# Optimization experiments

Measured on AMD Instinct MI355X. Metric: run time of the kernel, lower is better.

Reference implementation:

```python
import jax, jax.numpy as jnp
import numpy as np

K = 128
D = 256
N = 8192


def setup_inputs() -> dict:
    key = jax.random.key(0)
    k1, k2, k3, k4, k5 = jax.random.split(key, 5)
    x = jax.random.normal(k1, (N, D), dtype=jnp.float32)
    means = jax.random.uniform(k2, (K, D), dtype=jnp.float32)
    diag = 1.0 + 0.1 * jax.random.normal(k3, (1, K, D), dtype=jnp.float32)
    tri = 0.01 * jax.random.normal(k4, (1, K, D, D), dtype=jnp.float32)
    weigh = jax.random.normal(k5, (1, K), dtype=jnp.float32)
    return {"x": x, "means": means, "diag": diag, "tri": tri, "weigh": weigh}


def reference(x, means, diag, tri, weigh):
    # logC = -d/2 * log(2*pi)
    logC = jnp.asarray(-D / 2 * np.log(2 * np.pi), dtype=x.dtype)
    w = jax.nn.log_softmax(weigh, axis=1)            # [1, K]
    y = x[:, None, :] - means                        # [N, K, d]
    tril = jnp.tril(tri[0], k=-1)                    # [K, d, d] (strictly lower)
    # y * diag + batched tril matvec per component
    y = y * diag + jnp.einsum('kde,nke->nkd', tril, y)
    s = jnp.sum(y * y, axis=2)                       # [N, K]
    lp = -s / 2 + jnp.sum(jnp.log(jnp.abs(diag)), axis=2) + w  # [N, K]
    lp = jax.scipy.special.logsumexp(lp, axis=-1)    # [N]
    logpdf = logC + lp
    return jnp.mean(jnp.abs(-logpdf))
```

## Files before the change

### kernel.cpp

```cpp
#include <hip/hip_runtime.h>
#include <hip/hip_bf16.h>

#define DN   256
#define KC   128
#define NTOT 8192

typedef __attribute__((ext_vector_type(4)))  float f32x4;
typedef __attribute__((ext_vector_type(16))) float f32x16;
typedef __attribute__((ext_vector_type(4)))  unsigned int u32x4;
typedef __attribute__((ext_vector_type(8)))  int i32x8;

__device__ __forceinline__ unsigned pk4(float a0, float a1, float a2, float a3) {
  int v = __builtin_amdgcn_cvt_pk_fp8_f32(a0, a1, 0, false);
  v = __builtin_amdgcn_cvt_pk_fp8_f32(a2, a3, v, true);
  return (unsigned)v;
}
__device__ __forceinline__ float rt8(float v) {
  int p = __builtin_amdgcn_cvt_pk_fp8_f32(v, v, 0, false);
  return __builtin_amdgcn_cvt_f32_fp8(p, 0);
}

__device__ __forceinline__ void gload16(const void* g, void* l) {
  __builtin_amdgcn_global_load_lds(
      (const __attribute__((address_space(1))) unsigned int*)g,
      (__attribute__((address_space(3))) unsigned int*)l, 16, 0, 0);
}

__device__ __forceinline__ void inv_gran(int gi, int& r, int& g) {
  int l2 = gi >> 3, slot = gi & 7;
  int ss = slot ^ (l2 & 7);
  r = 2 * l2 + (ss >> 2);
  g = ss & 3;
}

__global__ void gmm_const(const float* __restrict__ diag,
                          const float* __restrict__ weigh,
                          float* __restrict__ ck) {
  int k = blockIdx.x;
  int lane = threadIdx.x;
  float w0 = weigh[lane], w1 = weigh[64 + lane];
  float mx = fmaxf(w0, w1);
#pragma unroll
  for (int off = 32; off > 0; off >>= 1) mx = fmaxf(mx, __shfl_xor(mx, off, 64));
  float s = expf(w0 - mx) + expf(w1 - mx);
#pragma unroll
  for (int off = 32; off > 0; off >>= 1) s += __shfl_xor(s, off, 64);
  float lse = mx + logf(s);
  float ld = 0.f;
  const float* dp = diag + (size_t)k * DN;
#pragma unroll
  for (int j = 0; j < 4; ++j) ld += logf(fabsf(dp[lane + 64 * j]));
#pragma unroll
  for (int off = 32; off > 0; off >>= 1) ld += __shfl_xor(ld, off, 64);
  if (lane == 0) ck[k] = ld + weigh[k] - lse;
}

__global__ void gmm_cvec(const float* __restrict__ tri,
                         const float* __restrict__ diag,
                         const float* __restrict__ means,
                         float* __restrict__ C) {
  int k  = blockIdx.x >> 2;
  int d0 = (blockIdx.x & 3) * 64;
  int lane = threadIdx.x & 63;
  int wid  = threadIdx.x >> 6;
  for (int i = 0; i < 16; ++i) {
    int d = d0 + wid * 16 + i;
    const float* trow = tri + (((size_t)k) << 16) + (d << 8);
    float dg = diag[(k << 8) + d];
    float acc = 0.f;
#pragma unroll
    for (int eb = 0; eb < DN; eb += 64) {
      int e = eb + lane;
      float mv = (e < d) ? trow[e] : ((e == d) ? dg : 0.f);
      acc += rt8(mv) * means[(k << 8) + e];
    }
#pragma unroll
    for (int off = 32; off > 0; off >>= 1) acc += __shfl_xor(acc, off, 64);
    if (lane == 0) C[(k << 8) + d] = acc;
  }
}

__global__ void gmm_packA(const float* __restrict__ x,
                          unsigned char* __restrict__ Xp) {
  int t = blockIdx.x * 256 + threadIdx.x;
  int rb = t >> 12;
  int rem = t & 4095;
  int tc = rem >> 10;
  int gi = rem & 1023;
  int r, g; inv_gran(gi, r, g);
  int row = rb * 256 + r;
  int e0 = tc * 64 + g * 16;
  const float* src = x + (size_t)row * DN + e0;
  float4 v0 = *(const float4*)src;
  float4 v1 = *(const float4*)(src + 4);
  float4 v2 = *(const float4*)(src + 8);
  float4 v3 = *(const float4*)(src + 12);
  u32x4 o = {pk4(v0.x, v0.y, v0.z, v0.w), pk4(v1.x, v1.y, v1.z, v1.w),
             pk4(v2.x, v2.y, v2.z, v2.w), pk4(v3.x, v3.y, v3.z, v3.w)};
  *(u32x4*)(Xp + (size_t)t * 16) = o;
}

__global__ void gmm_packB(const float* __restrict__ tri,
                          const float* __restrict__ diag,
                          unsigned char* __restrict__ Mp) {
  int t = blockIdx.x * 256 + threadIdx.x;
  int k = t >> 12;
  int rem = t & 4095;
  int tc = rem >> 10;
  int r2 = rem & 1023;
  int dhh = r2 >> 9;
  int gi = r2 & 511;
  int r, g; inv_gran(gi, r, g);
  int d = dhh * 128 + r;
  int e0 = tc * 64 + g * 16;
  const float* src = tri + (((size_t)k) << 16) + (d << 8) + e0;
  float dg = diag[(k << 8) + d];
  float4 v0 = *(const float4*)src;
  float4 v1 = *(const float4*)(src + 4);
  float4 v2 = *(const float4*)(src + 8);
  float4 v3 = *(const float4*)(src + 12);
  float f[16] = {v0.x, v0.y, v0.z, v0.w, v1.x, v1.y, v1.z, v1.w,
                 v2.x, v2.y, v2.z, v2.w, v3.x, v3.y, v3.z, v3.w};
#pragma unroll
  for (int j = 0; j < 16; ++j) {
    int e = e0 + j;
    f[j] = (e < d) ? f[j] : ((e == d) ? dg : 0.f);
  }
  u32x4 o = {pk4(f[0], f[1], f[2], f[3]), pk4(f[4], f[5], f[6], f[7]),
             pk4(f[8], f[9], f[10], f[11]), pk4(f[12], f[13], f[14], f[15])};
  *(u32x4*)(Mp + (size_t)t * 16) = o;
}

template <int USEP>
__global__ __launch_bounds__(512, 4) void gmm_gemm(
    const float* __restrict__ x, const float* __restrict__ tri,
    const float* __restrict__ diag, const unsigned char* __restrict__ Xp,
    const unsigned char* __restrict__ Mp, const float* __restrict__ C,
    float* __restrict__ Sp) {
  __shared__ __attribute__((aligned(16))) unsigned char As[3][8192];
  __shared__ __attribute__((aligned(16))) unsigned char Bs[3][16384];
  __shared__ float C_lds[128];
  __shared__ float spart[256][2];

  const int tid  = threadIdx.x;
  const int lane = tid & 63;
  const int wid  = tid >> 6;
  const int wm   = wid >> 1;
  const int wn   = wid & 1;
  const int l31  = lane & 31;
  const int h    = lane >> 5;

  const int bid = blockIdx.x;
  const int xcd = bid & 7;
  const int j   = bid >> 3;
  const int k   = xcd * 16 + (j & 15);
  const int u   = j >> 4;
  const int dh  = u & 1;
  const int rb  = u >> 1;
  const int NT  = 2 + 2 * dh;

  f32x16 acc[2][2];
#pragma unroll
  for (int df = 0; df < 2; ++df)
#pragma unroll
    for (int nf = 0; nf < 2; ++nf)
#pragma unroll
      for (int q = 0; q < 16; ++q) acc[df][nf][q] = 0.f;

  const int rA = wn * 32 + l31, lA = rA >> 1;
  const int rB = wm * 64 + l31, lB = rB >> 1;
  const int aoff0 = lA * 128 + (((2 * h)     + 4 * (rA & 1)) ^ (lA & 7)) * 16;
  const int aoff1 = lA * 128 + (((2 * h + 1) + 4 * (rA & 1)) ^ (lA & 7)) * 16;
  const int boff0 = lB * 128 + (((2 * h)     + 4 * (rB & 1)) ^ (lB & 7)) * 16;
  const int boff1 = lB * 128 + (((2 * h + 1) + 4 * (rB & 1)) ^ (lB & 7)) * 16;

  auto stage = [&](int ring, int tc) {
    gload16(Mp + (((size_t)((k * 4 + tc) * 2 + dh)) * 512 + tid) * 16,
            &As[ring][wid * 1024]);
    const unsigned char* gb = Xp + (((size_t)(rb * 4 + tc)) * 1024 + tid) * 16;
    gload16(gb, &Bs[ring][wid * 1024]);
    gload16(gb + 512 * 16, &Bs[ring][8192 + wid * 1024]);
  };

  auto compute = [&](int ring, int t) {
    const char* Ab = (const char*)&As[ring][0];
    const char* Bb = (const char*)&Bs[ring][0];
    u32x4 xlo[2], xhi[2];
#pragma unroll
    for (int nf = 0; nf < 2; ++nf) {
      xlo[nf] = *(const u32x4*)(Bb + boff0 + nf * 2048);
      xhi[nf] = *(const u32x4*)(Bb + boff1 + nf * 2048);
    }
#pragma unroll
    for (int df = 0; df < 2; ++df) {
      if (2 * dh + df >= t) {
        u32x4 m0 = *(const u32x4*)(Ab + aoff0 + df * 4096);
        u32x4 m1 = *(const u32x4*)(Ab + aoff1 + df * 4096);
        i32x8 ma;
#pragma unroll
        for (int q = 0; q < 4; ++q) { ma[q] = (int)m0[q]; ma[4 + q] = (int)m1[q]; }
#pragma unroll
        for (int nf = 0; nf < 2; ++nf) {
          i32x8 xb;
#pragma unroll
          for (int q = 0; q < 4; ++q) { xb[q] = (int)xlo[nf][q]; xb[4 + q] = (int)xhi[nf][q]; }
          acc[df][nf] = __builtin_amdgcn_mfma_scale_f32_32x32x64_f8f6f4(
              ma, xb, acc[df][nf], 0, 0, 0, 0x7f7f7f7f, 0, 0x7f7f7f7f);
        }
      }
    }
  };

  if (tid < 128) C_lds[tid] = C[(k << 8) + dh * 128 + tid];
  __syncthreads();

  if (USEP) {
    stage(0, 0); stage(1, 1);
    int rc = 0;
    for (int t = 0; t < NT; ++t) {
      if (t + 2 < NT) { int rs = rc + 2; if (rs >= 3) rs -= 3; stage(rs, t + 2); }
      int infl = NT - 1 - t; if (infl > 2) infl = 2;
      if (infl == 2)      asm volatile("s_waitcnt vmcnt(6)" ::: "memory");
      else if (infl == 1) asm volatile("s_waitcnt vmcnt(3)" ::: "memory");
      else                asm volatile("s_waitcnt vmcnt(0)" ::: "memory");
      __builtin_amdgcn_s_barrier();
      __builtin_amdgcn_sched_barrier(0);
      compute(rc, t);
      __builtin_amdgcn_s_barrier();
      __builtin_amdgcn_sched_barrier(0);
      if (++rc == 3) rc = 0;
    }
  } else {
    int rc = 0;
    for (int t = 0; t < NT; ++t) {
      __syncthreads();
      {
        int r, g; inv_gran(tid & 511, r, g);
        if (tid < 512) {
          int d = dh * 128 + r;
          int e0 = t * 64 + g * 16;
          const float* st = tri + (((size_t)k) << 16) + (d << 8) + e0;
          float dg = diag[(k << 8) + d];
          float f[16];
#pragma unroll
          for (int jj = 0; jj < 16; ++jj) {
            int e = e0 + jj;
            f[jj] = (e < d) ? st[jj] : ((e == d) ? dg : 0.f);
          }
          u32x4 o = {pk4(f[0], f[1], f[2], f[3]), pk4(f[4], f[5], f[6], f[7]),
                     pk4(f[8], f[9], f[10], f[11]), pk4(f[12], f[13], f[14], f[15])};
          *(u32x4*)&As[rc][(tid & 511) * 16] = o;
        }
      }
#pragma unroll
      for (int i = 0; i < 2; ++i) {
        int gi = i * 512 + tid;
        int r, g; inv_gran(gi, r, g);
        int row = rb * 256 + r;
        int e0 = t * 64 + g * 16;
        const float* sx = x + ((size_t)row << 8) + e0;
        float4 v0 = *(const float4*)sx;
        float4 v1 = *(const float4*)(sx + 4);
        float4 v2 = *(const float4*)(sx + 8);
        float4 v3 = *(const float4*)(sx + 12);
        u32x4 o = {pk4(v0.x, v0.y, v0.z, v0.w), pk4(v1.x, v1.y, v1.z, v1.w),
                   pk4(v2.x, v2.y, v2.z, v2.w), pk4(v3.x, v3.y, v3.z, v3.w)};
        *(u32x4*)&Bs[rc][gi * 16] = o;
      }
      __syncthreads();
      compute(rc, t);
      if (++rc == 3) rc = 0;
    }
    __syncthreads();
  }

  float s0 = 0.f, s1 = 0.f;
#pragma unroll
  for (int df = 0; df < 2; ++df)
#pragma unroll
    for (int qg = 0; qg < 4; ++qg) {
      f32x4 cv = *(const f32x4*)&C_lds[df * 64 + wn * 32 + qg * 8 + 4 * h];
#pragma unroll
      for (int qi = 0; qi < 4; ++qi) {
        int q = qg * 4 + qi;
        float z0 = acc[df][0][q] - cv[qi];
        float z1 = acc[df][1][q] - cv[qi];
        s0 += z0 * z0;
        s1 += z1 * z1;
      }
    }
  s0 += __shfl_xor(s0, 32, 64);
  s1 += __shfl_xor(s1, 32, 64);
  if (lane < 32) {
    spart[wm * 64 + l31][wn]      = s0;
    spart[wm * 64 + 32 + l31][wn] = s1;
  }
  __syncthreads();
  if (tid < 256)
    Sp[((size_t)(dh * KC + k)) * NTOT + rb * 256 + tid] =
        spart[tid][0] + spart[tid][1];
}

__global__ void gmm_lse(const float* __restrict__ Sp,
                        const float* __restrict__ ck,
                        float* __restrict__ out) {
  int n = blockIdx.x * 256 + threadIdx.x;
  float m = -1e30f, s = 0.f;
#pragma unroll 4
  for (int kk = 0; kk < KC; ++kk) {
    float sv = Sp[(size_t)kk * NTOT + n] + Sp[(size_t)(KC + kk) * NTOT + n];
    float v = ck[kk] - 0.5f * sv;
    float nm = fmaxf(m, v);
    s = s * expf(m - nm) + expf(v - nm);
    m = nm;
  }
  float lse = m + logf(s);
  const float logC = -(DN * 0.5f) * 1.8378770664093453f;
  float val = fabsf(logC + lse) * (1.0f / (float)NTOT);
  int lane = threadIdx.x & 63;
  int wid  = threadIdx.x >> 6;
#pragma unroll
  for (int off = 32; off > 0; off >>= 1) val += __shfl_down(val, off, 64);
  __shared__ float wsum[4];
  if (lane == 0) wsum[wid] = val;
  __syncthreads();
  if (threadIdx.x == 0)
    atomicAdd(out, wsum[0] + wsum[1] + wsum[2] + wsum[3]);
}

extern "C" void kernel_launch(void* const* d_in, const int* in_sizes, int n_in,
                              void* d_out, int out_size, void* d_ws, size_t ws_size,
                              hipStream_t stream) {
  const float* x     = (const float*)d_in[0];
  const float* means = (const float*)d_in[1];
  const float* diag  = (const float*)d_in[2];
  const float* tri   = (const float*)d_in[3];
  const float* weigh = (const float*)d_in[4];
  float* out = (float*)d_out;

  char* ws = (char*)d_ws;
  size_t off_ck = 0;
  size_t off_C  = 1024;
  size_t off_Sp = off_C + (size_t)KC * DN * 4;
  size_t off_Xp = off_Sp + (size_t)2 * KC * NTOT * 4;
  size_t off_Mp = off_Xp + (size_t)NTOT * DN;
  size_t need   = off_Mp + (size_t)KC * DN * DN;
  int useP = (ws_size >= need) ? 1 : 0;

  float* ck = (float*)(ws + off_ck);
  float* C  = (float*)(ws + off_C);
  float* Sp = (float*)(ws + off_Sp);
  unsigned char* Xp = (unsigned char*)(ws + off_Xp);
  unsigned char* Mp = (unsigned char*)(ws + off_Mp);

  hipMemsetAsync(d_out, 0, sizeof(float), stream);
  gmm_const<<<KC, 64, 0, stream>>>(diag, weigh, ck);
  gmm_cvec<<<KC * 4, 256, 0, stream>>>(tri, diag, means, C);
  if (useP) {
    gmm_packB<<<(KC * 4 * 2 * 512) / 256, 256, 0, stream>>>(tri, diag, Mp);
    gmm_packA<<<(32 * 4 * 1024) / 256, 256, 0, stream>>>(x, Xp);
    gmm_gemm<1><<<8192, 512, 0, stream>>>(x, tri, diag, Xp, Mp, C, Sp);
  } else {
    gmm_gemm<0><<<8192, 512, 0, stream>>>(x, tri, diag, Xp, Mp, C, Sp);
  }
  gmm_lse<<<NTOT / 256, 256, 0, stream>>>(Sp, ck, out);
}
```

Before: 116.6 us.

## Fuse prep kernels into one launch and compute C from packed fp8 tiles

```diff
diff --git a/kernel.cpp b/kernel.cpp
--- a/kernel.cpp
+++ b/kernel.cpp
@@ -33,102 +33,92 @@
   g = ss & 3;
 }
 
-__global__ void gmm_const(const float* __restrict__ diag,
-                          const float* __restrict__ weigh,
-                          float* __restrict__ ck) {
-  int k = blockIdx.x;
-  int lane = threadIdx.x;
-  float w0 = weigh[lane], w1 = weigh[64 + lane];
-  float mx = fmaxf(w0, w1);
-#pragma unroll
-  for (int off = 32; off > 0; off >>= 1) mx = fmaxf(mx, __shfl_xor(mx, off, 64));
-  float s = expf(w0 - mx) + expf(w1 - mx);
-#pragma unroll
-  for (int off = 32; off > 0; off >>= 1) s += __shfl_xor(s, off, 64);
-  float lse = mx + logf(s);
-  float ld = 0.f;
-  const float* dp = diag + (size_t)k * DN;
-#pragma unroll
-  for (int j = 0; j < 4; ++j) ld += logf(fabsf(dp[lane + 64 * j]));
-#pragma unroll
-  for (int off = 32; off > 0; off >>= 1) ld += __shfl_xor(ld, off, 64);
-  if (lane == 0) ck[k] = ld + weigh[k] - lse;
-}
-
-__global__ void gmm_cvec(const float* __restrict__ tri,
-                         const float* __restrict__ diag,
-                         const float* __restrict__ means,
-                         float* __restrict__ C) {
-  int k  = blockIdx.x >> 2;
-  int d0 = (blockIdx.x & 3) * 64;
-  int lane = threadIdx.x & 63;
-  int wid  = threadIdx.x >> 6;
-  for (int i = 0; i < 16; ++i) {
-    int d = d0 + wid * 16 + i;
-    const float* trow = tri + (((size_t)k) << 16) + (d << 8);
-    float dg = diag[(k << 8) + d];
-    float acc = 0.f;
-#pragma unroll
-    for (int eb = 0; eb < DN; eb += 64) {
-      int e = eb + lane;
-      float mv = (e < d) ? trow[e] : ((e == d) ? dg : 0.f);
-      acc += rt8(mv) * means[(k << 8) + e];
-    }
-#pragma unroll
-    for (int off = 32; off > 0; off >>= 1) acc += __shfl_xor(acc, off, 64);
-    if (lane == 0) C[(k << 8) + d] = acc;
-  }
-}
-
-__global__ void gmm_packA(const float* __restrict__ x,
-                          unsigned char* __restrict__ Xp) {
-  int t = blockIdx.x * 256 + threadIdx.x;
-  int rb = t >> 12;
-  int rem = t & 4095;
-  int tc = rem >> 10;
-  int gi = rem & 1023;
-  int r, g; inv_gran(gi, r, g);
-  int row = rb * 256 + r;
-  int e0 = tc * 64 + g * 16;
-  const float* src = x + (size_t)row * DN + e0;
-  float4 v0 = *(const float4*)src;
-  float4 v1 = *(const float4*)(src + 4);
-  float4 v2 = *(const float4*)(src + 8);
-  float4 v3 = *(const float4*)(src + 12);
-  u32x4 o = {pk4(v0.x, v0.y, v0.z, v0.w), pk4(v1.x, v1.y, v1.z, v1.w),
-             pk4(v2.x, v2.y, v2.z, v2.w), pk4(v3.x, v3.y, v3.z, v3.w)};
-  *(u32x4*)(Xp + (size_t)t * 16) = o;
-}
-
-__global__ void gmm_packB(const float* __restrict__ tri,
-                          const float* __restrict__ diag,
-                          unsigned char* __restrict__ Mp) {
-  int t = blockIdx.x * 256 + threadIdx.x;
-  int k = t >> 12;
-  int rem = t & 4095;
-  int tc = rem >> 10;
-  int r2 = rem & 1023;
-  int dhh = r2 >> 9;
-  int gi = r2 & 511;
-  int r, g; inv_gran(gi, r, g);
-  int d = dhh * 128 + r;
-  int e0 = tc * 64 + g * 16;
-  const float* src = tri + (((size_t)k) << 16) + (d << 8) + e0;
-  float dg = diag[(k << 8) + d];
-  float4 v0 = *(const float4*)src;
-  float4 v1 = *(const float4*)(src + 4);
-  float4 v2 = *(const float4*)(src + 8);
-  float4 v3 = *(const float4*)(src + 12);
-  float f[16] = {v0.x, v0.y, v0.z, v0.w, v1.x, v1.y, v1.z, v1.w,
-                 v2.x, v2.y, v2.z, v2.w, v3.x, v3.y, v3.z, v3.w};
-#pragma unroll
-  for (int j = 0; j < 16; ++j) {
-    int e = e0 + j;
-    f[j] = (e < d) ? f[j] : ((e == d) ? dg : 0.f);
-  }
-  u32x4 o = {pk4(f[0], f[1], f[2], f[3]), pk4(f[4], f[5], f[6], f[7]),
-             pk4(f[8], f[9], f[10], f[11]), pk4(f[12], f[13], f[14], f[15])};
-  *(u32x4*)(Mp + (size_t)t * 16) = o;
+__global__ __launch_bounds__(256) void gmm_prep(
+    const float* __restrict__ x, const float* __restrict__ tri,
+    const float* __restrict__ diag, const float* __restrict__ means,
+    const float* __restrict__ weigh,
+    unsigned char* __restrict__ Xp, unsigned char* __restrict__ Mp,
+    float* __restrict__ C, float* __restrict__ ck) {
+  int b = blockIdx.x;
+  if (b < 2048) {
+    int t = b * 256 + (int)threadIdx.x;
+    int k = t >> 12;
+    int rem = t & 4095;
+    int tc = rem >> 10;
+    int r2 = rem & 1023;
+    int dhh = r2 >> 9;
+    int gi = r2 & 511;
+    int r, g; inv_gran(gi, r, g);
+    int d = dhh * 128 + r;
+    int e0 = tc * 64 + g * 16;
+    if (e0 > d) {
+      u32x4 o = {0u, 0u, 0u, 0u};
+      *(u32x4*)(Mp + (size_t)t * 16) = o;
+    } else {
+      const float* src = tri + (((size_t)k) << 16) + (d << 8) + e0;
+      float dg = diag[(k << 8) + d];
+      float4 v0 = *(const float4*)src;
+      float4 v1 = *(const float4*)(src + 4);
+      float4 v2 = *(const float4*)(src + 8);
+      float4 v3 = *(const float4*)(src + 12);
+      float f[16] = {v0.x, v0.y, v0.z, v0.w, v1.x, v1.y, v1.z, v1.w,
+                     v2.x, v2.y, v2.z, v2.w, v3.x, v3.y, v3.z, v3.w};
+#pragma unroll
+      for (int jj = 0; jj < 16; ++jj) {
+        int e = e0 + jj;
+        f[jj] = (e < d) ? f[jj] : ((e == d) ? dg : 0.f);
+      }
+      u32x4 o = {pk4(f[0], f[1], f[2], f[3]), pk4(f[4], f[5], f[6], f[7]),
+                 pk4(f[8], f[9], f[10], f[11]), pk4(f[12], f[13], f[14], f[15])};
+      *(u32x4*)(Mp + (size_t)t * 16) = o;
+      float part = 0.f;
+      const float* mrow = means + (k << 8) + e0;
+#pragma unroll
+      for (int w = 0; w < 4; ++w) {
+        float4 mv = *(const float4*)(mrow + 4 * w);
+        part += __builtin_amdgcn_cvt_f32_fp8((int)o[w], 0) * mv.x;
+        part += __builtin_amdgcn_cvt_f32_fp8((int)o[w], 1) * mv.y;
+        part += __builtin_amdgcn_cvt_f32_fp8((int)o[w], 2) * mv.z;
+        part += __builtin_amdgcn_cvt_f32_fp8((int)o[w], 3) * mv.w;
+      }
+      atomicAdd(&C[(k << 8) + d], part);
+    }
+  } else if (b < 2560) {
+    int t = (b - 2048) * 256 + (int)threadIdx.x;
+    int rb = t >> 12;
+    int rem = t & 4095;
+    int tc = rem >> 10;
+    int gi = rem & 1023;
+    int r, g; inv_gran(gi, r, g);
+    int row = rb * 256 + r;
+    int e0 = tc * 64 + g * 16;
+    const float* src = x + (size_t)row * DN + e0;
+    float4 v0 = *(const float4*)src;
+    float4 v1 = *(const float4*)(src + 4);
+    float4 v2 = *(const float4*)(src + 8);
+    float4 v3 = *(const float4*)(src + 12);
+    u32x4 o = {pk4(v0.x, v0.y, v0.z, v0.w), pk4(v1.x, v1.y, v1.z, v1.w),
+               pk4(v2.x, v2.y, v2.z, v2.w), pk4(v3.x, v3.y, v3.z, v3.w)};
+    *(u32x4*)(Xp + (size_t)t * 16) = o;
+  } else {
+    int lane = (int)threadIdx.x & 63;
+    int kk = (b - 2560) * 4 + ((int)threadIdx.x >> 6);
+    float w0 = weigh[lane], w1 = weigh[64 + lane];
+    float mx = fmaxf(w0, w1);
+#pragma unroll
+    for (int off = 32; off > 0; off >>= 1) mx = fmaxf(mx, __shfl_xor(mx, off, 64));
+    float s = expf(w0 - mx) + expf(w1 - mx);
+#pragma unroll
+    for (int off = 32; off > 0; off >>= 1) s += __shfl_xor(s, off, 64);
+    float lse = mx + logf(s);
+    float ld = 0.f;
+    const float* dp = diag + (size_t)kk * DN;
+#pragma unroll
+    for (int jj = 0; jj < 4; ++jj) ld += logf(fabsf(dp[lane + 64 * jj]));
+#pragma unroll
+    for (int off = 32; off > 0; off >>= 1) ld += __shfl_xor(ld, off, 64);
+    if (lane == 0) ck[kk] = ld + weigh[kk] - lse;
+  }
 }
 
 template <int USEP>
@@ -328,6 +318,53 @@
     atomicAdd(out, wsum[0] + wsum[1] + wsum[2] + wsum[3]);
 }
 
+__global__ void gmm_const(const float* __restrict__ diag,
+                          const float* __restrict__ weigh,
+                          float* __restrict__ ck) {
+  int k = blockIdx.x;
+  int lane = threadIdx.x;
+  float w0 = weigh[lane], w1 = weigh[64 + lane];
+  float mx = fmaxf(w0, w1);
+#pragma unroll
+  for (int off = 32; off > 0; off >>= 1) mx = fmaxf(mx, __shfl_xor(mx, off, 64));
+  float s = expf(w0 - mx) + expf(w1 - mx);
+#pragma unroll
+  for (int off = 32; off > 0; off >>= 1) s += __shfl_xor(s, off, 64);
+  float lse = mx + logf(s);
+  float ld = 0.f;
+  const float* dp = diag + (size_t)k * DN;
+#pragma unroll
+  for (int j = 0; j < 4; ++j) ld += logf(fabsf(dp[lane + 64 * j]));
+#pragma unroll
+  for (int off = 32; off > 0; off >>= 1) ld += __shfl_xor(ld, off, 64);
+  if (lane == 0) ck[k] = ld + weigh[k] - lse;
+}
+
+__global__ void gmm_cvec(const float* __restrict__ tri,
+                         const float* __restrict__ diag,
+                         const float* __restrict__ means,
+                         float* __restrict__ C) {
+  int k  = blockIdx.x >> 2;
+  int d0 = (blockIdx.x & 3) * 64;
+  int lane = threadIdx.x & 63;
+  int wid  = threadIdx.x >> 6;
+  for (int i = 0; i < 16; ++i) {
+    int d = d0 + wid * 16 + i;
+    const float* trow = tri + (((size_t)k) << 16) + (d << 8);
+    float dg = diag[(k << 8) + d];
+    float acc = 0.f;
+#pragma unroll
+    for (int eb = 0; eb < DN; eb += 64) {
+      int e = eb + lane;
+      float mv = (e < d) ? trow[e] : ((e == d) ? dg : 0.f);
+      acc += rt8(mv) * means[(k << 8) + e];
+    }
+#pragma unroll
+    for (int off = 32; off > 0; off >>= 1) acc += __shfl_xor(acc, off, 64);
+    if (lane == 0) C[(k << 8) + d] = acc;
+  }
+}
+
 extern "C" void kernel_launch(void* const* d_in, const int* in_sizes, int n_in,
                               void* d_out, int out_size, void* d_ws, size_t ws_size,
                               hipStream_t stream) {
@@ -354,13 +391,13 @@
   unsigned char* Mp = (unsigned char*)(ws + off_Mp);
 
   hipMemsetAsync(d_out, 0, sizeof(float), stream);
-  gmm_const<<<KC, 64, 0, stream>>>(diag, weigh, ck);
-  gmm_cvec<<<KC * 4, 256, 0, stream>>>(tri, diag, means, C);
   if (useP) {
-    gmm_packB<<<(KC * 4 * 2 * 512) / 256, 256, 0, stream>>>(tri, diag, Mp);
-    gmm_packA<<<(32 * 4 * 1024) / 256, 256, 0, stream>>>(x, Xp);
+    hipMemsetAsync(C, 0, (size_t)KC * DN * 4, stream);
+    gmm_prep<<<2592, 256, 0, stream>>>(x, tri, diag, means, weigh, Xp, Mp, C, ck);
     gmm_gemm<1><<<8192, 512, 0, stream>>>(x, tri, diag, Xp, Mp, C, Sp);
   } else {
+    gmm_const<<<KC, 64, 0, stream>>>(diag, weigh, ck);
+    gmm_cvec<<<KC * 4, 256, 0, stream>>>(tri, diag, means, C);
     gmm_gemm<0><<<8192, 512, 0, stream>>>(x, tri, diag, Xp, Mp, C, Sp);
   }
   gmm_lse<<<NTOT / 256, 256, 0, stream>>>(Sp, ck, out);
```

Measured after the change: 124.6 us. 6.9% more time.

## Merge both d-halves into one block to reuse X tiles across full D

Applied to the files above, without the earlier changes.

```diff
diff --git a/kernel.cpp b/kernel.cpp
--- a/kernel.cpp
+++ b/kernel.cpp
@@ -113,6 +113,11 @@
   int r, g; inv_gran(gi, r, g);
   int d = dhh * 128 + r;
   int e0 = tc * 64 + g * 16;
+  if (e0 > d) {
+    u32x4 o = {0u, 0u, 0u, 0u};
+    *(u32x4*)(Mp + (size_t)t * 16) = o;
+    return;
+  }
   const float* src = tri + (((size_t)k) << 16) + (d << 8) + e0;
   float dg = diag[(k << 8) + d];
   float4 v0 = *(const float4*)src;
@@ -132,21 +137,21 @@
 }
 
 template <int USEP>
-__global__ __launch_bounds__(512, 4) void gmm_gemm(
+__global__ __launch_bounds__(512, 2) void gmm_gemm(
     const float* __restrict__ x, const float* __restrict__ tri,
     const float* __restrict__ diag, const unsigned char* __restrict__ Xp,
     const unsigned char* __restrict__ Mp, const float* __restrict__ C,
     float* __restrict__ Sp) {
-  __shared__ __attribute__((aligned(16))) unsigned char As[3][8192];
+  __shared__ __attribute__((aligned(16))) unsigned char As[3][16384];
   __shared__ __attribute__((aligned(16))) unsigned char Bs[3][16384];
-  __shared__ float C_lds[128];
+  __shared__ float C_lds[256];
   __shared__ float spart[256][2];
 
   const int tid  = threadIdx.x;
   const int lane = tid & 63;
   const int wid  = tid >> 6;
   const int wm   = wid >> 1;
-  const int wn   = wid & 1;
+  const int ws   = wid & 1;
   const int l31  = lane & 31;
   const int h    = lane >> 5;
 
@@ -154,20 +159,18 @@
   const int xcd = bid & 7;
   const int j   = bid >> 3;
   const int k   = xcd * 16 + (j & 15);
-  const int u   = j >> 4;
-  const int dh  = u & 1;
-  const int rb  = u >> 1;
-  const int NT  = 2 + 2 * dh;
-
-  f32x16 acc[2][2];
-#pragma unroll
-  for (int df = 0; df < 2; ++df)
+  const int rb  = j >> 4;
+  const int NT  = 4;
+
+  f32x16 acc[4][2];
+#pragma unroll
+  for (int fi = 0; fi < 4; ++fi)
 #pragma unroll
     for (int nf = 0; nf < 2; ++nf)
 #pragma unroll
-      for (int q = 0; q < 16; ++q) acc[df][nf][q] = 0.f;
-
-  const int rA = wn * 32 + l31, lA = rA >> 1;
+      for (int q = 0; q < 16; ++q) acc[fi][nf][q] = 0.f;
+
+  const int rA = ws * 32 + l31, lA = rA >> 1;
   const int rB = wm * 64 + l31, lB = rB >> 1;
   const int aoff0 = lA * 128 + (((2 * h)     + 4 * (rA & 1)) ^ (lA & 7)) * 16;
   const int aoff1 = lA * 128 + (((2 * h + 1) + 4 * (rA & 1)) ^ (lA & 7)) * 16;
@@ -175,11 +178,12 @@
   const int boff1 = lB * 128 + (((2 * h + 1) + 4 * (rB & 1)) ^ (lB & 7)) * 16;
 
   auto stage = [&](int ring, int tc) {
-    gload16(Mp + (((size_t)((k * 4 + tc) * 2 + dh)) * 512 + tid) * 16,
-            &As[ring][wid * 1024]);
+    const unsigned char* ga = Mp + (((size_t)(k * 4 + tc)) * 1024 + tid) * 16;
+    gload16(ga, &As[ring][wid * 1024]);
+    gload16(ga + 8192, &As[ring][8192 + wid * 1024]);
     const unsigned char* gb = Xp + (((size_t)(rb * 4 + tc)) * 1024 + tid) * 16;
     gload16(gb, &Bs[ring][wid * 1024]);
-    gload16(gb + 512 * 16, &Bs[ring][8192 + wid * 1024]);
+    gload16(gb + 8192, &Bs[ring][8192 + wid * 1024]);
   };
 
   auto compute = [&](int ring, int t) {
@@ -192,10 +196,10 @@
       xhi[nf] = *(const u32x4*)(Bb + boff1 + nf * 2048);
     }
 #pragma unroll
-    for (int df = 0; df < 2; ++df) {
-      if (2 * dh + df >= t) {
-        u32x4 m0 = *(const u32x4*)(Ab + aoff0 + df * 4096);
-        u32x4 m1 = *(const u32x4*)(Ab + aoff1 + df * 4096);
+    for (int fi = 0; fi < 4; ++fi) {
+      if (fi >= t) {
+        u32x4 m0 = *(const u32x4*)(Ab + aoff0 + fi * 4096);
+        u32x4 m1 = *(const u32x4*)(Ab + aoff1 + fi * 4096);
         i32x8 ma;
 #pragma unroll
         for (int q = 0; q < 4; ++q) { ma[q] = (int)m0[q]; ma[4 + q] = (int)m1[q]; }
@@ -204,14 +208,14 @@
           i32x8 xb;
 #pragma unroll
           for (int q = 0; q < 4; ++q) { xb[q] = (int)xlo[nf][q]; xb[4 + q] = (int)xhi[nf][q]; }
-          acc[df][nf] = __builtin_amdgcn_mfma_scale_f32_32x32x64_f8f6f4(
-              ma, xb, acc[df][nf], 0, 0, 0, 0x7f7f7f7f, 0, 0x7f7f7f7f);
+          acc[fi][nf] = __builtin_amdgcn_mfma_scale_f32_32x32x64_f8f6f4(
+              ma, xb, acc[fi][nf], 0, 0, 0, 0x7f7f7f7f, 0, 0x7f7f7f7f);
         }
       }
     }
   };
 
-  if (tid < 128) C_lds[tid] = C[(k << 8) + dh * 128 + tid];
+  if (tid < 256) C_lds[tid] = C[(k << 8) + tid];
   __syncthreads();
 
   if (USEP) {
@@ -220,8 +224,8 @@
     for (int t = 0; t < NT; ++t) {
       if (t + 2 < NT) { int rs = rc + 2; if (rs >= 3) rs -= 3; stage(rs, t + 2); }
       int infl = NT - 1 - t; if (infl > 2) infl = 2;
-      if (infl == 2)      asm volatile("s_waitcnt vmcnt(6)" ::: "memory");
-      else if (infl == 1) asm volatile("s_waitcnt vmcnt(3)" ::: "memory");
+      if (infl == 2)      asm volatile("s_waitcnt vmcnt(8)" ::: "memory");
+      else if (infl == 1) asm volatile("s_waitcnt vmcnt(4)" ::: "memory");
       else                asm volatile("s_waitcnt vmcnt(0)" ::: "memory");
       __builtin_amdgcn_s_barrier();
       __builtin_amdgcn_sched_barrier(0);
@@ -234,23 +238,29 @@
     int rc = 0;
     for (int t = 0; t < NT; ++t) {
       __syncthreads();
-      {
-        int r, g; inv_gran(tid & 511, r, g);
-        if (tid < 512) {
-          int d = dh * 128 + r;
-          int e0 = t * 64 + g * 16;
+#pragma unroll
+      for (int i = 0; i < 2; ++i) {
+        int gi = i * 512 + tid;
+        int half = gi >> 9;
+        int r, g; inv_gran(gi & 511, r, g);
+        int d = half * 128 + r;
+        int e0 = t * 64 + g * 16;
+        float f[16];
+        if (e0 > d) {
+#pragma unroll
+          for (int jj = 0; jj < 16; ++jj) f[jj] = 0.f;
+        } else {
           const float* st = tri + (((size_t)k) << 16) + (d << 8) + e0;
           float dg = diag[(k << 8) + d];
-          float f[16];
 #pragma unroll
           for (int jj = 0; jj < 16; ++jj) {
             int e = e0 + jj;
             f[jj] = (e < d) ? st[jj] : ((e == d) ? dg : 0.f);
           }
-          u32x4 o = {pk4(f[0], f[1], f[2], f[3]), pk4(f[4], f[5], f[6], f[7]),
-                     pk4(f[8], f[9], f[10], f[11]), pk4(f[12], f[13], f[14], f[15])};
-          *(u32x4*)&As[rc][(tid & 511) * 16] = o;
         }
+        u32x4 o = {pk4(f[0], f[1], f[2], f[3]), pk4(f[4], f[5], f[6], f[7]),
+                   pk4(f[8], f[9], f[10], f[11]), pk4(f[12], f[13], f[14], f[15])};
+        *(u32x4*)&As[rc][gi * 16] = o;
       }
 #pragma unroll
       for (int i = 0; i < 2; ++i) {
@@ -276,15 +286,15 @@
 
   float s0 = 0.f, s1 = 0.f;
 #pragma unroll
-  for (int df = 0; df < 2; ++df)
+  for (int fi = 0; fi < 4; ++fi)
 #pragma unroll
     for (int qg = 0; qg < 4; ++qg) {
-      f32x4 cv = *(const f32x4*)&C_lds[df * 64 + wn * 32 + qg * 8 + 4 * h];
+      f32x4 cv = *(const f32x4*)&C_lds[ws * 32 + fi * 64 + qg * 8 + 4 * h];
 #pragma unroll
       for (int qi = 0; qi < 4; ++qi) {
         int q = qg * 4 + qi;
-        float z0 = acc[df][0][q] - cv[qi];
-        float z1 = acc[df][1][q] - cv[qi];
+        float z0 = acc[fi][0][q] - cv[qi];
+        float z1 = acc[fi][1][q] - cv[qi];
         s0 += z0 * z0;
         s1 += z1 * z1;
       }
@@ -292,13 +302,14 @@
   s0 += __shfl_xor(s0, 32, 64);
   s1 += __shfl_xor(s1, 32, 64);
   if (lane < 32) {
-    spart[wm * 64 + l31][wn]      = s0;
-    spart[wm * 64 + 32 + l31][wn] = s1;
+    spart[wm * 64 + l31][ws]      = s0;
+    spart[wm * 64 + 32 + l31][ws] = s1;
   }
   __syncthreads();
-  if (tid < 256)
-    Sp[((size_t)(dh * KC + k)) * NTOT + rb * 256 + tid] =
-        spart[tid][0] + spart[tid][1];
+  if (tid < 256) {
+    Sp[(size_t)k * NTOT + rb * 256 + tid]              = spart[tid][0];
+    Sp[((size_t)(KC + k)) * NTOT + rb * 256 + tid]     = spart[tid][1];
+  }
 }
 
 __global__ void gmm_lse(const float* __restrict__ Sp,
@@ -359,9 +370,9 @@
   if (useP) {
     gmm_packB<<<(KC * 4 * 2 * 512) / 256, 256, 0, stream>>>(tri, diag, Mp);
     gmm_packA<<<(32 * 4 * 1024) / 256, 256, 0, stream>>>(x, Xp);
-    gmm_gemm<1><<<8192, 512, 0, stream>>>(x, tri, diag, Xp, Mp, C, Sp);
+    gmm_gemm<1><<<4096, 512, 0, stream>>>(x, tri, diag, Xp, Mp, C, Sp);
   } else {
-    gmm_gemm<0><<<8192, 512, 0, stream>>>(x, tri, diag, Xp, Mp, C, Sp);
+    gmm_gemm<0><<<4096, 512, 0, stream>>>(x, tri, diag, Xp, Mp, C, Sp);
   }
   gmm_lse<<<NTOT / 256, 256, 0, stream>>>(Sp, ck, out);
 }
```

New measurement: 122.0 us. 4.7% more time.
